# Kernel tuning notes

Measured on AMD Instinct MI355X. Metric: run time of the kernel, lower is better.

Reference implementation:

```python
import jax, jax.numpy as jnp
import numpy as np

B, H, N, DN, G = 16, 512, 2048, 256, 64
LN_EPS = 1e-5
DEG_EPS = 1e-8


def setup_inputs() -> dict:
    key = jax.random.key(0)
    ks = jax.random.split(key, 8)
    s = lambda fan_in: 1.0 / np.sqrt(fan_in)
    return {
        "h_t": jax.random.normal(ks[0], (B, H), jnp.float32),
        "node_repr": jax.random.normal(ks[1], (N, DN), jnp.float32),
        "base_adj": jax.random.uniform(ks[2], (N, N), jnp.float32),
        "Wq": jax.random.normal(ks[3], (G, H), jnp.float32) * s(H),
        "bq": jnp.zeros((G,), jnp.float32),
        "Wk": jax.random.normal(ks[4], (G, DN), jnp.float32) * s(DN),
        "bk": jnp.zeros((G,), jnp.float32),
        "Wv": jax.random.normal(ks[5], (G, DN), jnp.float32) * s(DN),
        "bv": jnp.zeros((G,), jnp.float32),
        "Wo": jax.random.normal(ks[6], (G, G), jnp.float32) * s(G),
        "bo": jnp.zeros((G,), jnp.float32),
        "gamma": jnp.ones((G,), jnp.float32),
        "beta": jnp.zeros((G,), jnp.float32),
    }


def reference(h_t, node_repr, base_adj, Wq, bq, Wk, bk, Wv, bv, Wo, bo, gamma, beta):
    g = Wq.shape[0]
    q = h_t @ Wq.T + bq                      # [B,G]
    k = node_repr @ Wk.T + bk                # [N,G]
    v = node_repr @ Wv.T + bv                # [N,G]
    logits = (q @ k.T) / (g ** 0.5)          # [B,N]
    alpha = jax.nn.softmax(logits, axis=-1)  # [B,N] (dropout is identity in eval)
    relation_vector = alpha @ v              # [B,G]

    n = base_adj.shape[0]
    # dynamic adjacency with self loops: [B,N,N]
    A = alpha[:, :, None] * base_adj[None, :, :] + jnp.eye(n, dtype=base_adj.dtype)
    # symmetric normalization D^{-1/2} A D^{-1/2}, batched as a broadcast
    d_inv_sqrt = (A.sum(axis=-1) + DEG_EPS) ** -0.5            # [B,N]
    A_norm = d_inv_sqrt[:, :, None] * A * d_inv_sqrt[:, None, :]

    z = jnp.einsum('bnm,mg->bng', A_norm, v)  # propagate
    z = z @ Wo.T + bo
    z = jax.nn.relu(z)
    mu = z.mean(axis=-1, keepdims=True)
    var = ((z - mu) ** 2).mean(axis=-1, keepdims=True)
    updated_nodes = (z - mu) * jax.lax.rsqrt(var + LN_EPS) * gamma + beta  # [B,N,G]

    propagated_summary = jnp.einsum('bn,bng->bg', alpha, updated_nodes)
    return propagated_summary, relation_vector, updated_nodes
```

## Files before the change

kernel.cpp:

```cpp
#include <hip/hip_runtime.h>
#include <hip/hip_bf16.h>
#include <cstddef>
#include <cstdint>

#define B_ 16
#define H_ 512
#define N_ 2048
#define DN_ 256
#define G_ 64

typedef __attribute__((ext_vector_type(8))) short short8;
typedef __attribute__((ext_vector_type(4))) short s16x4;
typedef __attribute__((ext_vector_type(4))) float f32x4;

__device__ __forceinline__ unsigned short f2bf(float x) {
    __hip_bfloat16 b = __float2bfloat16(x);
    return *(unsigned short*)&b;
}

__device__ __forceinline__ short8 pack8(f32x4 a, f32x4 b) {
    short8 r;
    r[0] = (short)f2bf(a[0]); r[1] = (short)f2bf(a[1]);
    r[2] = (short)f2bf(a[2]); r[3] = (short)f2bf(a[3]);
    r[4] = (short)f2bf(b[0]); r[5] = (short)f2bf(b[1]);
    r[6] = (short)f2bf(b[2]); r[7] = (short)f2bf(b[3]);
    return r;
}

__device__ __forceinline__ void gl_lds16(const void* g, void* l) {
    __builtin_amdgcn_global_load_lds(
        (const __attribute__((address_space(1))) unsigned int*)g,
        (__attribute__((address_space(3))) unsigned int*)l, 16, 0, 0);
}

static constexpr size_t OFF_Q      = 0;
static constexpr size_t OFF_KT     = 4096;
static constexpr size_t OFF_V      = OFF_KT + (size_t)N_*G_*4;
static constexpr size_t OFF_ALPHA  = OFF_V + (size_t)N_*G_*4;
static constexpr size_t OFF_DIS    = OFF_ALPHA + (size_t)B_*N_*4;
static constexpr size_t OFF_ROWSUM = OFF_DIS + (size_t)B_*N_*4;
static constexpr size_t OFF_ABF    = OFF_ROWSUM + 8192;
static constexpr size_t OFF_VPT    = OFF_ABF + (size_t)N_*N_*2;

__global__ __launch_bounds__(256) void prep_kernel(const float* __restrict__ h_t,
                                                   const float* __restrict__ Wq,
                                                   const float* __restrict__ bq,
                                                   const float* __restrict__ node_repr,
                                                   const float* __restrict__ Wk,
                                                   const float* __restrict__ bk,
                                                   const float* __restrict__ Wv,
                                                   const float* __restrict__ bv,
                                                   const float* __restrict__ base_adj,
                                                   float* __restrict__ q,
                                                   float* __restrict__ kT,
                                                   float* __restrict__ v,
                                                   __hip_bfloat16* __restrict__ Abf,
                                                   float* __restrict__ rowsum,
                                                   float* __restrict__ out) {
    __shared__ __align__(16) short smem[16384];
    const int bid = blockIdx.x, tid = threadIdx.x;
    const int wave = tid >> 6, l = tid & 63;
    const int lr = l & 15, kg = l >> 4;
    if (bid < 16) {
        short* Xs = smem;
        short* Ws = smem + 8192;
        const int n0 = bid * 128;
        f32x4 acc[2][8];
        #pragma unroll
        for (int fr = 0; fr < 2; fr++)
            #pragma unroll
            for (int fc = 0; fc < 8; fc++) acc[fr][fc] = (f32x4){0.f, 0.f, 0.f, 0.f};
        for (int kt = 0; kt < 4; kt++) {
            __syncthreads();
            #pragma unroll
            for (int j = 0; j < 4; j++) {
                int c = tid + j * 256;
                int row = c >> 3, c16 = c & 7;
                const float* src = node_repr + (size_t)(n0 + row) * DN_ + kt * 64 + c16 * 8;
                *(short8*)&Xs[(row * 8 + (c16 ^ (row & 7))) * 8] =
                    pack8(*(const f32x4*)src, *(const f32x4*)(src + 4));
            }
            #pragma unroll
            for (int j = 0; j < 4; j++) {
                int c = tid + j * 256;
                int row = c >> 3, c16 = c & 7;
                const float* src = (row < 64)
                    ? (Wk + (size_t)row * DN_ + kt * 64 + c16 * 8)
                    : (Wv + (size_t)(row - 64) * DN_ + kt * 64 + c16 * 8);
                *(short8*)&Ws[(row * 8 + (c16 ^ (row & 7))) * 8] =
                    pack8(*(const f32x4*)src, *(const f32x4*)(src + 4));
            }
            __syncthreads();
            #pragma unroll
            for (int ks = 0; ks < 2; ks++) {
                short8 af[2], bf[8];
                #pragma unroll
                for (int fr = 0; fr < 2; fr++) {
                    int row = wave * 32 + fr * 16 + lr;
                    af[fr] = *(const short8*)&Xs[(row * 8 + ((ks * 4 + kg) ^ (row & 7))) * 8];
                }
                #pragma unroll
                for (int fc = 0; fc < 8; fc++) {
                    int row = fc * 16 + lr;
                    bf[fc] = *(const short8*)&Ws[(row * 8 + ((ks * 4 + kg) ^ (row & 7))) * 8];
                }
                #pragma unroll
                for (int fr = 0; fr < 2; fr++)
                    #pragma unroll
                    for (int fc = 0; fc < 8; fc++)
                        acc[fr][fc] = __builtin_amdgcn_mfma_f32_16x16x32_bf16(af[fr], bf[fc], acc[fr][fc], 0, 0, 0);
            }
        }
        #pragma unroll
        for (int fr = 0; fr < 2; fr++) {
            int nb = n0 + wave * 32 + fr * 16 + kg * 4;
            #pragma unroll
            for (int fc = 0; fc < 4; fc++) {
                int cc = fc * 16 + lr;
                float bias = bk[cc];
                f32x4 o;
                o[0] = acc[fr][fc][0] + bias; o[1] = acc[fr][fc][1] + bias;
                o[2] = acc[fr][fc][2] + bias; o[3] = acc[fr][fc][3] + bias;
                *(f32x4*)&kT[(size_t)cc * N_ + nb] = o;
            }
            #pragma unroll
            for (int fc = 4; fc < 8; fc++) {
                int cv = fc * 16 + lr - 64;
                float bias = bv[cv];
                #pragma unroll
                for (int r = 0; r < 4; r++)
                    v[(size_t)(nb + r) * G_ + cv] = acc[fr][fc][r] + bias;
            }
        }
    } else if (bid == 16) {
        #pragma unroll
        for (int j = 0; j < 8; j++) out[tid + j * 256] = 0.f;
        short* Hs = smem;
        short* Wqs = smem + 2048;
        f32x4 acc[4];
        #pragma unroll
        for (int fc = 0; fc < 4; fc++) acc[fc] = (f32x4){0.f, 0.f, 0.f, 0.f};
        for (int kt = 0; kt < 4; kt++) {
            __syncthreads();
            {
                int row = tid >> 4, c16 = tid & 15;
                const float* src = h_t + (size_t)row * H_ + kt * 128 + c16 * 8;
                *(short8*)&Hs[(row * 16 + (c16 ^ (row & 7))) * 8] =
                    pack8(*(const f32x4*)src, *(const f32x4*)(src + 4));
            }
            #pragma unroll
            for (int j = 0; j < 4; j++) {
                int c = tid + j * 256;
                int row = c >> 4, c16 = c & 15;
                const float* src = Wq + (size_t)row * H_ + kt * 128 + c16 * 8;
                *(short8*)&Wqs[(row * 16 + (c16 ^ (row & 7))) * 8] =
                    pack8(*(const f32x4*)src, *(const f32x4*)(src + 4));
            }
            __syncthreads();
            if (wave == 0) {
                #pragma unroll
                for (int ks = 0; ks < 4; ks++) {
                    short8 af = *(const short8*)&Hs[(lr * 16 + ((ks * 4 + kg) ^ (lr & 7))) * 8];
                    #pragma unroll
                    for (int fc = 0; fc < 4; fc++) {
                        int row = fc * 16 + lr;
                        short8 bf = *(const short8*)&Wqs[(row * 16 + ((ks * 4 + kg) ^ (row & 7))) * 8];
                        acc[fc] = __builtin_amdgcn_mfma_f32_16x16x32_bf16(af, bf, acc[fc], 0, 0, 0);
                    }
                }
            }
        }
        if (wave == 0) {
            #pragma unroll
            for (int fc = 0; fc < 4; fc++) {
                int gcol = fc * 16 + lr;
                float bias = bq[gcol];
                #pragma unroll
                for (int r = 0; r < 4; r++)
                    q[(kg * 4 + r) * G_ + gcol] = acc[fc][r] + bias;
            }
        }
    } else {
        const int n = (bid - 17) * 4 + wave;
        const f32x4* src = (const f32x4*)(base_adj + (size_t)n * N_);
        s16x4* dst = (s16x4*)(Abf + (size_t)n * N_);
        float s = 0.f;
        #pragma unroll
        for (int i = 0; i < 8; i++) {
            int m4 = l + i * 64;
            f32x4 x = src[m4];
            s += x[0] + x[1] + x[2] + x[3];
            s16x4 o;
            o[0] = (short)f2bf(x[0]); o[1] = (short)f2bf(x[1]);
            o[2] = (short)f2bf(x[2]); o[3] = (short)f2bf(x[3]);
            dst[m4] = o;
        }
        #pragma unroll
        for (int off = 32; off; off >>= 1) s += __shfl_xor(s, off, 64);
        if (l == 0) rowsum[n] = s;
    }
}

__global__ __launch_bounds__(1024) void attn_kernel(const float* __restrict__ q,
                                                    const float* __restrict__ kT,
                                                    const float* __restrict__ rowsum,
                                                    const float* __restrict__ v,
                                                    float* __restrict__ alpha,
                                                    float* __restrict__ dis,
                                                    __hip_bfloat16* __restrict__ VpT,
                                                    float* __restrict__ out) {
    __shared__ float qs[G_];
    __shared__ float red[16];
    __shared__ float bval;
    __shared__ float als[N_];
    __shared__ float dss[N_];
    __shared__ float vs[64 * 65];
    const int b = blockIdx.x, chunk = blockIdx.y, tid = threadIdx.x;
    if (tid < G_) qs[tid] = q[b * G_ + tid];
    __syncthreads();
    int n1 = tid, n2 = tid + 1024;
    float l1 = 0.f, l2 = 0.f;
    #pragma unroll 8
    for (int g = 0; g < G_; g++) {
        float qq = qs[g];
        l1 = fmaf(qq, kT[(size_t)g * N_ + n1], l1);
        l2 = fmaf(qq, kT[(size_t)g * N_ + n2], l2);
    }
    l1 *= 0.125f; l2 *= 0.125f;
    float m = fmaxf(l1, l2);
    #pragma unroll
    for (int off = 32; off; off >>= 1) m = fmaxf(m, __shfl_xor(m, off, 64));
    if ((tid & 63) == 0) red[tid >> 6] = m;
    __syncthreads();
    if (tid < 16) {
        float x = red[tid];
        #pragma unroll
        for (int off = 8; off; off >>= 1) x = fmaxf(x, __shfl_xor(x, off, 16));
        if (tid == 0) bval = x;
    }
    __syncthreads();
    m = bval;
    __syncthreads();
    float e1 = expf(l1 - m), e2 = expf(l2 - m);
    float s = e1 + e2;
    #pragma unroll
    for (int off = 32; off; off >>= 1) s += __shfl_xor(s, off, 64);
    if ((tid & 63) == 0) red[tid >> 6] = s;
    __syncthreads();
    if (tid < 16) {
        float x = red[tid];
        #pragma unroll
        for (int off = 8; off; off >>= 1) x += __shfl_xor(x, off, 16);
        if (tid == 0) bval = x;
    }
    __syncthreads();
    float inv = 1.f / bval;
    float a1 = e1 * inv, a2 = e2 * inv;
    float d1 = rsqrtf(fmaf(a1, rowsum[n1], 1.f + 1e-8f));
    float d2 = rsqrtf(fmaf(a2, rowsum[n2], 1.f + 1e-8f));
    if (chunk == 0) {
        alpha[(size_t)b * N_ + n1] = a1;
        alpha[(size_t)b * N_ + n2] = a2;
        dis[(size_t)b * N_ + n1] = d1;
        dis[(size_t)b * N_ + n2] = d2;
    }
    als[n1] = a1; als[n2] = a2;
    dss[n1] = d1; dss[n2] = d2;

    float relacc = 0.f;
    const int gg = tid >> 4, mq = (tid & 15) * 4;
    #pragma unroll
    for (int sub = 0; sub < 4; sub++) {
        const int m0 = chunk * 256 + sub * 64;
        __syncthreads();
        {
            int mm = tid >> 4, g4 = (tid & 15) << 2;
            f32x4 x = *(const f32x4*)&v[(size_t)(m0 + mm) * G_ + g4];
            vs[mm * 65 + g4 + 0] = x[0];
            vs[mm * 65 + g4 + 1] = x[1];
            vs[mm * 65 + g4 + 2] = x[2];
            vs[mm * 65 + g4 + 3] = x[3];
        }
        __syncthreads();
        s16x4 pk;
        #pragma unroll
        for (int j = 0; j < 4; j++) {
            int mm = mq + j;
            float vv = vs[mm * 65 + gg];
            pk[j] = (short)f2bf(dss[m0 + mm] * vv);
            relacc = fmaf(als[m0 + mm], vv, relacc);
        }
        *(s16x4*)&VpT[((size_t)b * G_ + gg) * N_ + m0 + mq] = pk;
    }
    __syncthreads();
    vs[tid] = relacc;
    __syncthreads();
    if (tid < G_) {
        float r = 0.f;
        #pragma unroll
        for (int i = 0; i < 16; i++) r += vs[tid * 16 + i];
        atomicAdd(&out[1024 + b * G_ + tid], r);
    }
}

#define BM 64
#define BN 64
#define BK 128
#define NKT (N_ / BK)
__global__ __launch_bounds__(256) void gemm_fused(const __hip_bfloat16* __restrict__ Abf,
                                                  const __hip_bfloat16* __restrict__ VpT,
                                                  const float* __restrict__ v,
                                                  const float* __restrict__ alpha,
                                                  const float* __restrict__ dis,
                                                  const float* __restrict__ Wo,
                                                  const float* __restrict__ bo,
                                                  const float* __restrict__ gamma,
                                                  const float* __restrict__ beta,
                                                  float* __restrict__ un,
                                                  float* __restrict__ outp) {
    __shared__ __align__(16) short A_lds[2][BM * BK];
    __shared__ __align__(16) short B_lds[2][BN * BK];
    __shared__ float ad_s[2][BM];
    __shared__ float psum_w[4][G_];
    const int tid = threadIdx.x;
    const int wg = blockIdx.x;
    const int xcd = wg & 7, c = wg >> 3;
    const int n0 = (c >> 1) * BM;
    const int b = xcd * 2 + (c & 1);
    const int c0 = b * BN;
    const int wave = tid >> 6, l = tid & 63;
    const int wr = wave >> 1, wc = wave & 1;
    const int lr = l & 15, kg = l >> 4;

    if (tid < BM) {
        ad_s[0][tid] = alpha[(size_t)b * N_ + n0 + tid];
        ad_s[1][tid] = dis[(size_t)b * N_ + n0 + tid];
    }

    f32x4 acc[2][2];
    #pragma unroll
    for (int m = 0; m < 2; m++)
        #pragma unroll
        for (int n = 0; n < 2; n++) acc[m][n] = (f32x4){0.f, 0.f, 0.f, 0.f};

    const int srow = tid >> 4;
    const int c16 = tid & 15;
    const int scol = ((c16 & 8) | ((c16 ^ srow) & 7)) << 3;
    const __hip_bfloat16* ag = Abf + (size_t)(n0 + srow) * N_ + scol;
    const __hip_bfloat16* bg = VpT + (size_t)(c0 + srow) * N_ + scol;

    #define STAGE(buf, kpos)                                                  \
        do {                                                                  \
            _Pragma("unroll")                                                 \
            for (int j = 0; j < 4; j++)                                       \
                gl_lds16(ag + (size_t)j * 16 * N_ + (kpos),                   \
                         &A_lds[buf][(wave * 4 + j * 16) * BK]);              \
            _Pragma("unroll")                                                 \
            for (int j = 0; j < 4; j++)                                       \
                gl_lds16(bg + (size_t)j * 16 * N_ + (kpos),                   \
                         &B_lds[buf][(wave * 4 + j * 16) * BK]);              \
        } while (0)

    STAGE(0, 0);
    __syncthreads();

    int cur = 0;
    for (int t = 0; t < NKT; t++) {
        if (t + 1 < NKT) STAGE(cur ^ 1, (t + 1) * BK);
        #pragma unroll
        for (int ks = 0; ks < 4; ks++) {
            const int chunk = ks * 4 + kg;
            short8 av[2], bv2[2];
            #pragma unroll
            for (int m = 0; m < 2; m++) {
                int row = wr * 32 + m * 16 + lr;
                int swc = (chunk & 8) | ((chunk ^ lr) & 7);
                av[m] = *(const short8*)&A_lds[cur][row * BK + swc * 8];
            }
            #pragma unroll
            for (int n = 0; n < 2; n++) {
                int row = wc * 32 + n * 16 + lr;
                int swc = (chunk & 8) | ((chunk ^ lr) & 7);
                bv2[n] = *(const short8*)&B_lds[cur][row * BK + swc * 8];
            }
            #pragma unroll
            for (int m = 0; m < 2; m++)
                #pragma unroll
                for (int n = 0; n < 2; n++)
                    acc[m][n] = __builtin_amdgcn_mfma_f32_16x16x32_bf16(av[m], bv2[n], acc[m][n], 0, 0, 0);
        }
        __syncthreads();
        cur ^= 1;
    }
    #undef STAGE

    unsigned short* z_s = (unsigned short*)&A_lds[0][0];
    uint32_t* wo_s = (uint32_t*)&A_lds[1][0];

    {
        int g = tid >> 2;
        int j0 = (tid & 3) * 16;
        #pragma unroll
        for (int jj = 0; jj < 8; jj++) {
            int g2 = j0 + jj * 2;
            uint32_t pk = (uint32_t)f2bf(Wo[g * G_ + g2]) |
                          ((uint32_t)f2bf(Wo[g * G_ + g2 + 1]) << 16);
            int dwc = ((g2 >> 1) ^ ((g & 7) << 2)) & 31;
            wo_s[g * 32 + dwc] = pk;
        }
    }
    #pragma unroll
    for (int m = 0; m < 2; m++)
        #pragma unroll
        for (int nn = 0; nn < 2; nn++)
            #pragma unroll
            for (int r = 0; r < 4; r++) {
                int row = wr * 32 + m * 16 + kg * 4 + r;
                int g2 = wc * 32 + nn * 16 + lr;
                float al = ad_s[0][row], di = ad_s[1][row];
                float vv = v[(size_t)(n0 + row) * G_ + g2];
                float zp = di * fmaf(al, acc[m][nn][r], di * vv);
                int dwc = ((g2 >> 1) ^ (((row >> 2) & 3) << 3)) & 31;
                z_s[(row * 32 + dwc) * 2 + (g2 & 1)] = f2bf(zp);
            }
    float bo_l[4], ga_l[4], be_l[4];
    #pragma unroll
    for (int ct = 0; ct < 4; ct++) {
        bo_l[ct] = bo[ct * 16 + lr];
        ga_l[ct] = gamma[ct * 16 + lr];
        be_l[ct] = beta[ct * 16 + lr];
    }
    __syncthreads();

    short8 aw[2], bw[4][2];
    #pragma unroll
    for (int kh = 0; kh < 2; kh++) {
        int arow = wave * 16 + lr;
        int dwc = ((kh * 16 + kg * 4) ^ (((arow >> 2) & 3) << 3)) & 31;
        aw[kh] = *(const short8*)&z_s[(arow * 32 + dwc) * 2];
    }
    #pragma unroll
    for (int ct = 0; ct < 4; ct++) {
        int col = ct * 16 + lr;
        #pragma unroll
        for (int kh = 0; kh < 2; kh++) {
            int dwc = ((kh * 16 + kg * 4) ^ ((col & 7) << 2)) & 31;
            bw[ct][kh] = *(const short8*)&((unsigned short*)wo_s)[(col * 32 + dwc) * 2];
        }
    }
    f32x4 acc2[4];
    #pragma unroll
    for (int ct = 0; ct < 4; ct++) acc2[ct] = (f32x4){0.f, 0.f, 0.f, 0.f};
    #pragma unroll
    for (int kh = 0; kh < 2; kh++)
        #pragma unroll
        for (int ct = 0; ct < 4; ct++)
            acc2[ct] = __builtin_amdgcn_mfma_f32_16x16x32_bf16(aw[kh], bw[ct][kh], acc2[ct], 0, 0, 0);

    float psum_l[4] = {0.f, 0.f, 0.f, 0.f};
    #pragma unroll
    for (int rr = 0; rr < 4; rr++) {
        int lrow = wave * 16 + kg * 4 + rr;
        float y[4], s = 0.f;
        #pragma unroll
        for (int ct = 0; ct < 4; ct++) {
            y[ct] = fmaxf(acc2[ct][rr] + bo_l[ct], 0.f);
            s += y[ct];
        }
        s += __shfl_xor(s, 1, 64); s += __shfl_xor(s, 2, 64);
        s += __shfl_xor(s, 4, 64); s += __shfl_xor(s, 8, 64);
        float mu = s * (1.f / 64.f);
        float s2 = 0.f;
        #pragma unroll
        for (int ct = 0; ct < 4; ct++) { float d = y[ct] - mu; s2 += d * d; }
        s2 += __shfl_xor(s2, 1, 64); s2 += __shfl_xor(s2, 2, 64);
        s2 += __shfl_xor(s2, 4, 64); s2 += __shfl_xor(s2, 8, 64);
        float rstd = rsqrtf(s2 * (1.f / 64.f) + 1e-5f);
        float al = ad_s[0][lrow];
        size_t ubase = ((size_t)b * N_ + n0 + lrow) * G_;
        #pragma unroll
        for (int ct = 0; ct < 4; ct++) {
            float outv = fmaf((y[ct] - mu) * rstd, ga_l[ct], be_l[ct]);
            un[ubase + ct * 16 + lr] = outv;
            psum_l[ct] = fmaf(al, outv, psum_l[ct]);
        }
    }
    #pragma unroll
    for (int ct = 0; ct < 4; ct++) {
        psum_l[ct] += __shfl_xor(psum_l[ct], 16, 64);
        psum_l[ct] += __shfl_xor(psum_l[ct], 32, 64);
    }
    if (kg == 0)
        #pragma unroll
        for (int ct = 0; ct < 4; ct++) psum_w[wave][ct * 16 + lr] = psum_l[ct];
    __syncthreads();
    if (tid < G_) {
        float p = psum_w[0][tid] + psum_w[1][tid] + psum_w[2][tid] + psum_w[3][tid];
        atomicAdd(&outp[b * G_ + tid], p);
    }
}

extern "C" void kernel_launch(void* const* d_in, const int* in_sizes, int n_in,
                              void* d_out, int out_size, void* d_ws, size_t ws_size,
                              hipStream_t stream) {
    const float* h_t       = (const float*)d_in[0];
    const float* node_repr = (const float*)d_in[1];
    const float* base_adj  = (const float*)d_in[2];
    const float* Wq    = (const float*)d_in[3];
    const float* bq    = (const float*)d_in[4];
    const float* Wk    = (const float*)d_in[5];
    const float* bk    = (const float*)d_in[6];
    const float* Wv    = (const float*)d_in[7];
    const float* bv    = (const float*)d_in[8];
    const float* Wo    = (const float*)d_in[9];
    const float* bo    = (const float*)d_in[10];
    const float* gamma = (const float*)d_in[11];
    const float* beta  = (const float*)d_in[12];
    float* out = (float*)d_out;

    char* ws = (char*)d_ws;
    float* q      = (float*)(ws + OFF_Q);
    float* kT     = (float*)(ws + OFF_KT);
    float* v      = (float*)(ws + OFF_V);
    float* alpha  = (float*)(ws + OFF_ALPHA);
    float* dis    = (float*)(ws + OFF_DIS);
    float* rowsum = (float*)(ws + OFF_ROWSUM);
    __hip_bfloat16* Abf = (__hip_bfloat16*)(ws + OFF_ABF);
    __hip_bfloat16* VpT = (__hip_bfloat16*)(ws + OFF_VPT);

    float* un = out + 2048;

    prep_kernel<<<17 + 512, 256, 0, stream>>>(h_t, Wq, bq, node_repr, Wk, bk,
                                              Wv, bv, base_adj, q, kT, v, Abf, rowsum, out);
    attn_kernel<<<dim3(B_, 8), 1024, 0, stream>>>(q, kT, rowsum, v, alpha, dis, VpT, out);
    gemm_fused<<<(N_ / BM) * (B_ * G_ / BN), 256, 0, stream>>>(Abf, VpT, v, alpha, dis,
                                                               Wo, bo, gamma, beta, un, out);
}
```

Measured before the change: 52.34 us.

## Split GEMM K-dimension across waves with LDS reduction instead of output tiling

The main GEMM loop now gives each wave a quarter of every K tile, and each wave computes the full 64x64 output block. Previously each wave owned a 32x32 output quadrant. After the loop, the four partial accumulators are written to LDS and summed so that each wave ends up with its 16 rows for the epilogue. LDS is now one raw byte buffer that is reused for the reduction. The aim is fewer LDS fragment reads per MFMA: each wave reads 8 fragments per K tile and issues 16 MFMAs, against 16 reads for the same 16 MFMAs before. The cost is 64 accumulator registers per thread plus an extra LDS reduction pass with two barriers.

After: 48.95 us. 6.5% less time.

```diff
diff --git a/kernel.cpp b/kernel.cpp
--- a/kernel.cpp
+++ b/kernel.cpp
@@ -318,10 +318,9 @@
                                                   const float* __restrict__ beta,
                                                   float* __restrict__ un,
                                                   float* __restrict__ outp) {
-    __shared__ __align__(16) short A_lds[2][BM * BK];
-    __shared__ __align__(16) short B_lds[2][BN * BK];
-    __shared__ float ad_s[2][BM];
-    __shared__ float psum_w[4][G_];
+    __shared__ __align__(16) char smem[65536 + 1536];
+    float* ad_s = (float*)(smem + 65536);
+    float* psum_w = (float*)(smem + 66048);
     const int tid = threadIdx.x;
     const int wg = blockIdx.x;
     const int xcd = wg & 7, c = wg >> 3;
@@ -329,73 +328,86 @@
     const int b = xcd * 2 + (c & 1);
     const int c0 = b * BN;
     const int wave = tid >> 6, l = tid & 63;
-    const int wr = wave >> 1, wc = wave & 1;
     const int lr = l & 15, kg = l >> 4;
 
     if (tid < BM) {
-        ad_s[0][tid] = alpha[(size_t)b * N_ + n0 + tid];
-        ad_s[1][tid] = dis[(size_t)b * N_ + n0 + tid];
-    }
-
-    f32x4 acc[2][2];
-    #pragma unroll
-    for (int m = 0; m < 2; m++)
-        #pragma unroll
-        for (int n = 0; n < 2; n++) acc[m][n] = (f32x4){0.f, 0.f, 0.f, 0.f};
+        ad_s[tid] = alpha[(size_t)b * N_ + n0 + tid];
+        ad_s[64 + tid] = dis[(size_t)b * N_ + n0 + tid];
+    }
+
+    f32x4 acc[4][4];
+    #pragma unroll
+    for (int m = 0; m < 4; m++)
+        #pragma unroll
+        for (int n = 0; n < 4; n++) acc[m][n] = (f32x4){0.f, 0.f, 0.f, 0.f};
 
     const int srow = tid >> 4;
-    const int c16 = tid & 15;
-    const int scol = ((c16 & 8) | ((c16 ^ srow) & 7)) << 3;
+    const int c16s = tid & 15;
+    const int scol = ((c16s & 8) | ((c16s ^ srow) & 7)) << 3;
     const __hip_bfloat16* ag = Abf + (size_t)(n0 + srow) * N_ + scol;
     const __hip_bfloat16* bg = VpT + (size_t)(c0 + srow) * N_ + scol;
 
-    #define STAGE(buf, kpos)                                                  \
+    #define STAGE(bufidx, kpos)                                               \
         do {                                                                  \
+            short* Ad = (short*)(smem + (bufidx) * 16384);                    \
+            short* Bd = (short*)(smem + 32768 + (bufidx) * 16384);            \
             _Pragma("unroll")                                                 \
             for (int j = 0; j < 4; j++)                                       \
                 gl_lds16(ag + (size_t)j * 16 * N_ + (kpos),                   \
-                         &A_lds[buf][(wave * 4 + j * 16) * BK]);              \
+                         &Ad[(wave * 4 + j * 16) * BK]);                      \
             _Pragma("unroll")                                                 \
             for (int j = 0; j < 4; j++)                                       \
                 gl_lds16(bg + (size_t)j * 16 * N_ + (kpos),                   \
-                         &B_lds[buf][(wave * 4 + j * 16) * BK]);              \
+                         &Bd[(wave * 4 + j * 16) * BK]);                      \
         } while (0)
 
     STAGE(0, 0);
     __syncthreads();
 
+    const int chunk = wave * 4 + kg;
+    const int swc = ((chunk & 8) | ((chunk ^ lr) & 7)) * 8;
     int cur = 0;
     for (int t = 0; t < NKT; t++) {
         if (t + 1 < NKT) STAGE(cur ^ 1, (t + 1) * BK);
-        #pragma unroll
-        for (int ks = 0; ks < 4; ks++) {
-            const int chunk = ks * 4 + kg;
-            short8 av[2], bv2[2];
-            #pragma unroll
-            for (int m = 0; m < 2; m++) {
-                int row = wr * 32 + m * 16 + lr;
-                int swc = (chunk & 8) | ((chunk ^ lr) & 7);
-                av[m] = *(const short8*)&A_lds[cur][row * BK + swc * 8];
-            }
-            #pragma unroll
-            for (int n = 0; n < 2; n++) {
-                int row = wc * 32 + n * 16 + lr;
-                int swc = (chunk & 8) | ((chunk ^ lr) & 7);
-                bv2[n] = *(const short8*)&B_lds[cur][row * BK + swc * 8];
-            }
-            #pragma unroll
-            for (int m = 0; m < 2; m++)
-                #pragma unroll
-                for (int n = 0; n < 2; n++)
-                    acc[m][n] = __builtin_amdgcn_mfma_f32_16x16x32_bf16(av[m], bv2[n], acc[m][n], 0, 0, 0);
-        }
+        const short* Ab = (const short*)(smem + cur * 16384);
+        const short* Bb = (const short*)(smem + 32768 + cur * 16384);
+        short8 av[4], bv2[4];
+        #pragma unroll
+        for (int m = 0; m < 4; m++)
+            av[m] = *(const short8*)&Ab[(m * 16 + lr) * BK + swc];
+        #pragma unroll
+        for (int n = 0; n < 4; n++)
+            bv2[n] = *(const short8*)&Bb[(n * 16 + lr) * BK + swc];
+        #pragma unroll
+        for (int m = 0; m < 4; m++)
+            #pragma unroll
+            for (int n = 0; n < 4; n++)
+                acc[m][n] = __builtin_amdgcn_mfma_f32_16x16x32_bf16(av[m], bv2[n], acc[m][n], 0, 0, 0);
         __syncthreads();
         cur ^= 1;
     }
     #undef STAGE
 
-    unsigned short* z_s = (unsigned short*)&A_lds[0][0];
-    uint32_t* wo_s = (uint32_t*)&A_lds[1][0];
+    float* red = (float*)smem;
+    #pragma unroll
+    for (int m = 0; m < 4; m++)
+        #pragma unroll
+        for (int n = 0; n < 4; n++)
+            *(f32x4*)&red[((wave * 16 + m * 4 + n) * 64 + l) * 4] = acc[m][n];
+    __syncthreads();
+    f32x4 cfin[4];
+    #pragma unroll
+    for (int n = 0; n < 4; n++) {
+        f32x4 s0 = *(const f32x4*)&red[((0 + wave * 4 + n) * 64 + l) * 4];
+        f32x4 s1 = *(const f32x4*)&red[((16 + wave * 4 + n) * 64 + l) * 4];
+        f32x4 s2 = *(const f32x4*)&red[((32 + wave * 4 + n) * 64 + l) * 4];
+        f32x4 s3 = *(const f32x4*)&red[((48 + wave * 4 + n) * 64 + l) * 4];
+        cfin[n] = (s0 + s1) + (s2 + s3);
+    }
+    __syncthreads();
+
+    unsigned short* z_s = (unsigned short*)smem;
+    uint32_t* wo_s = (uint32_t*)(smem + 32768);
 
     {
         int g = tid >> 2;
@@ -410,19 +422,17 @@
         }
     }
     #pragma unroll
-    for (int m = 0; m < 2; m++)
-        #pragma unroll
-        for (int nn = 0; nn < 2; nn++)
-            #pragma unroll
-            for (int r = 0; r < 4; r++) {
-                int row = wr * 32 + m * 16 + kg * 4 + r;
-                int g2 = wc * 32 + nn * 16 + lr;
-                float al = ad_s[0][row], di = ad_s[1][row];
-                float vv = v[(size_t)(n0 + row) * G_ + g2];
-                float zp = di * fmaf(al, acc[m][nn][r], di * vv);
-                int dwc = ((g2 >> 1) ^ (((row >> 2) & 3) << 3)) & 31;
-                z_s[(row * 32 + dwc) * 2 + (g2 & 1)] = f2bf(zp);
-            }
+    for (int nn = 0; nn < 4; nn++)
+        #pragma unroll
+        for (int r = 0; r < 4; r++) {
+            int row = wave * 16 + kg * 4 + r;
+            int g2 = nn * 16 + lr;
+            float al = ad_s[row], di = ad_s[64 + row];
+            float vv = v[(size_t)(n0 + row) * G_ + g2];
+            float zp = di * fmaf(al, cfin[nn][r], di * vv);
+            int dwc = ((g2 >> 1) ^ (((row >> 2) & 3) << 3)) & 31;
+            z_s[(row * 32 + dwc) * 2 + (g2 & 1)] = f2bf(zp);
+        }
     float bo_l[4], ga_l[4], be_l[4];
     #pragma unroll
     for (int ct = 0; ct < 4; ct++) {
@@ -476,7 +486,7 @@
         s2 += __shfl_xor(s2, 1, 64); s2 += __shfl_xor(s2, 2, 64);
         s2 += __shfl_xor(s2, 4, 64); s2 += __shfl_xor(s2, 8, 64);
         float rstd = rsqrtf(s2 * (1.f / 64.f) + 1e-5f);
-        float al = ad_s[0][lrow];
+        float al = ad_s[lrow];
         size_t ubase = ((size_t)b * N_ + n0 + lrow) * G_;
         #pragma unroll
         for (int ct = 0; ct < 4; ct++) {
@@ -492,10 +502,10 @@
     }
     if (kg == 0)
         #pragma unroll
-        for (int ct = 0; ct < 4; ct++) psum_w[wave][ct * 16 + lr] = psum_l[ct];
+        for (int ct = 0; ct < 4; ct++) psum_w[wave * 64 + ct * 16 + lr] = psum_l[ct];
     __syncthreads();
     if (tid < G_) {
-        float p = psum_w[0][tid] + psum_w[1][tid] + psum_w[2][tid] + psum_w[3][tid];
+        float p = psum_w[tid] + psum_w[64 + tid] + psum_w[128 + tid] + psum_w[192 + tid];
         atomicAdd(&outp[b * G_ + tid], p);
     }
 }
```
